# Performance work log

Hardware: AMD Instinct MI355X
Metric: run time of the kernel (lower is better)

The kernel has to match this reference:

```python
import jax, jax.numpy as jnp
import numpy as np

EPS = 1e-8
NEG_INF = -jnp.inf


def setup_inputs() -> dict:
    key = jax.random.key(0)
    k1, k2, k3, k4 = jax.random.split(key, 4)
    B1, S1, B2, S2, H = 64, 128, 64, 128, 768
    x1 = jax.random.normal(k1, (B1, S1, H), dtype=jnp.float32)
    x2 = jax.random.normal(k2, (B2, S2, H), dtype=jnp.float32)
    mask1 = jax.random.randint(k3, (B1, S1), 0, 2).astype(jnp.int32)
    mask2 = jax.random.randint(k4, (B2, S2), 0, 2).astype(jnp.int32)
    # ensure at least one valid token per sequence
    mask1 = mask1.at[:, 0].set(1)
    mask2 = mask2.at[:, 0].set(1)
    return {"x1": x1, "mask1": mask1, "x2": x2, "mask2": mask2}


def _full_cosine(x1, x2):
    # x1: (B1,S1,H), x2: (B2,S2,H) -> sim: (B1,B2,S1,S2)
    n1 = jnp.linalg.norm(x1, axis=-1)  # (B1,S1)
    n2 = jnp.linalg.norm(x2, axis=-1)  # (B2,S2)
    dots = jnp.einsum('ash,bth->abst', x1, x2)
    denom = jnp.maximum(n1[:, None, :, None] * n2[None, :, None, :], EPS)
    return dots / denom


def _masked_mean(sim, mask, axis):
    m = mask.astype(bool)
    num = jnp.sum(jnp.where(m, sim, 0.0), axis=axis)
    den = jnp.sum(mask.astype(sim.dtype), axis=axis)
    return num / den


def reference(x1, mask1, x2, mask2):
    sim = _full_cosine(x1, x2)  # (B1,B2,S1,S2), unmasked cosine
    masked = jnp.where(mask1.astype(bool)[:, None, :, None], sim, NEG_INF)
    masked = jnp.where(mask2.astype(bool)[None, :, None, :], masked, NEG_INF)
    ind1 = jnp.argmax(masked, axis=-1)  # (B1,B2,S1): best x2 token per x1 token
    ind2 = jnp.argmax(masked, axis=-2)  # (B1,B2,S2): best x1 token per x2 token
    # gather unmasked cosine at the argmax indices (equivalent to recomputing
    # cosine on the gathered vectors as the torch code does)
    sim1 = jnp.take_along_axis(sim, ind1[..., None], axis=3)[..., 0]  # (B1,B2,S1)
    sim2 = jnp.take_along_axis(sim, ind2[..., None, :], axis=2)[..., 0, :]  # (B1,B2,S2)
    m1 = jnp.broadcast_to(mask1[:, None, :], sim1.shape)
    m2 = jnp.broadcast_to(mask2[None, :, :], sim2.shape)
    s1 = _masked_mean(sim1, m1, axis=-1)  # (B1,B2)
    s2 = _masked_mean(sim2, m2, axis=-1)  # (B1,B2)
    return (s1 + s2) / 2
```

## Files before the change

### kernel.cpp

```cpp
#include <hip/hip_runtime.h>
#include <hip/hip_bf16.h>

#define H_DIM 768
#define S_LEN 128
#define NT 12
#define MROWS 8192

typedef __attribute__((ext_vector_type(8))) short short8;
typedef __attribute__((ext_vector_type(4))) float f32x4;

__device__ __forceinline__ void gload_lds16(const void* g, void* l) {
  __builtin_amdgcn_global_load_lds(
      (const __attribute__((address_space(1))) unsigned int*)g,
      (__attribute__((address_space(3))) unsigned int*)l, 16, 0, 0);
}

__global__ __launch_bounds__(128) void prep_kernel(
    const int* __restrict__ mask1, const int* __restrict__ mask2,
    int* __restrict__ dest, int* __restrict__ cnts) {
  const int sq = blockIdx.x;
  const int* mask = (sq < 64) ? (mask1 + sq * S_LEN) : (mask2 + (sq - 64) * S_LEN);
  const int tid = threadIdx.x;
  const int lane = tid & 63, wv = tid >> 6;
  const int m = mask[tid] ? 1 : 0;
  const unsigned long long bal = __ballot(m);
  const int pre = __popcll(bal & ((1ull << lane) - 1ull));
  __shared__ int wsum[2];
  if (lane == 0) wsum[wv] = __popcll(bal);
  __syncthreads();
  const int base = (wv == 1) ? wsum[0] : 0;
  dest[sq * S_LEN + tid] = m ? (base + pre) : -1;
  if (tid == 0) cnts[sq] = wsum[0] + wsum[1];
}

__global__ __launch_bounds__(512) void scan_kernel(
    const int* __restrict__ cnts, int* __restrict__ off1, int* __restrict__ off2,
    unsigned* __restrict__ vbitsM, unsigned* __restrict__ vbitsN,
    int* __restrict__ dims) {
  __shared__ int so1[65], so2[65];
  const int tid = threadIdx.x;
  const int lane = tid & 63, wv = tid >> 6;
  if (tid < 128) {
    const int* cb = (wv == 0) ? cnts : (cnts + 64);
    const int np = (cb[lane] + 15) & ~15;
    int inc = np;
#pragma unroll
    for (int o = 1; o < 64; o <<= 1) {
      const int t = __shfl_up(inc, o);
      if (lane >= o) inc += t;
    }
    int* so = wv ? so2 : so1;
    so[lane] = inc - np;
    if (lane == 63) so[64] = inc;
  }
  __syncthreads();
  const int Mtot = so1[64], Ntot = so2[64];
  if (tid == 0) {
    const int Mpad = (Mtot + 127) & ~127, Npad = (Ntot + 127) & ~127;
    dims[0] = Mpad; dims[1] = Npad; dims[2] = Mpad >> 7; dims[3] = Npad >> 7;
  }
  if (tid < 65) { off1[tid] = so1[tid]; off2[tid] = so2[tid]; }
  unsigned bm = 0, bn = 0;
  const int r0 = tid * 16;
  if (r0 < Mtot) {
    int s = 0;
    while (so1[s + 1] <= r0) ++s;
    const int b0 = so1[s], nv = cnts[s];
#pragma unroll
    for (int k = 0; k < 16; ++k)
      if (r0 + k - b0 < nv) bm |= (1u << k);
  }
  if (r0 < Ntot) {
    int s = 0;
    while (so2[s + 1] <= r0) ++s;
    const int b0 = so2[s], nv = cnts[64 + s];
#pragma unroll
    for (int k = 0; k < 16; ++k)
      if (r0 + k - b0 < nv) bn |= (1u << k);
  }
  vbitsM[tid] = bm;
  vbitsN[tid] = bn;
}

__global__ __launch_bounds__(256) void normzero_kernel(
    const float* __restrict__ x1, const float* __restrict__ x2,
    const int* __restrict__ dest, const int* __restrict__ off1,
    const int* __restrict__ off2,
    const unsigned* __restrict__ vbitsM, const unsigned* __restrict__ vbitsN,
    const int* __restrict__ dims,
    unsigned short* __restrict__ xc1, unsigned short* __restrict__ xc2) {
  const int gid = blockIdx.x;
  const int tid = threadIdx.x;
  if (gid >= 16384) {
    const int row = gid - 16384;
    if (tid < 96) {
      const short8 z8 = (short8){0, 0, 0, 0, 0, 0, 0, 0};
      if (row < dims[0] && !((vbitsM[row >> 4] >> (row & 15)) & 1u))
        reinterpret_cast<short8*>(xc1 + (size_t)row * H_DIM)[tid] = z8;
      if (row < dims[1] && !((vbitsN[row >> 4] >> (row & 15)) & 1u))
        reinterpret_cast<short8*>(xc2 + (size_t)row * H_DIM)[tid] = z8;
    }
    return;
  }
  const int sg = gid >> 7, tok = gid & 127;
  const int d = dest[sg * S_LEN + tok];
  if (d < 0) return;
  const bool is1 = (gid < 8192);
  const float* row = is1 ? (x1 + (size_t)gid * H_DIM)
                         : (x2 + (size_t)(gid - 8192) * H_DIM);
  const int grow = (is1 ? off1[sg] : off2[sg - 64]) + d;
  unsigned short* orow = (is1 ? xc1 : xc2) + (size_t)grow * H_DIM;
  float4 v = make_float4(0.f, 0.f, 0.f, 0.f);
  float ss = 0.f;
  if (tid < 192) {
    v = reinterpret_cast<const float4*>(row)[tid];
    ss = v.x * v.x + v.y * v.y + v.z * v.z + v.w * v.w;
  }
#pragma unroll
  for (int o = 32; o > 0; o >>= 1) ss += __shfl_down(ss, o);
  __shared__ float ws[4];
  if ((tid & 63) == 0) ws[tid >> 6] = ss;
  __syncthreads();
  const float scale = 1.0f / sqrtf(ws[0] + ws[1] + ws[2] + ws[3]);
  if (tid < 192) {
    union { ushort4 u; __hip_bfloat16 h[4]; } o;
    o.h[0] = __float2bfloat16(v.x * scale);
    o.h[1] = __float2bfloat16(v.y * scale);
    o.h[2] = __float2bfloat16(v.z * scale);
    o.h[3] = __float2bfloat16(v.w * scale);
    reinterpret_cast<ushort4*>(orow)[tid] = o.u;
  }
}

__global__ __launch_bounds__(256, 4) void gemm_kernel(
    const unsigned short* __restrict__ xc1, const unsigned short* __restrict__ xc2,
    const unsigned* __restrict__ vbitsM, const unsigned* __restrict__ vbitsN,
    const int* __restrict__ dims,
    float* __restrict__ rowgranT, float* __restrict__ colgranT) {
  __shared__ __align__(16) unsigned short Al[128 * 64];
  __shared__ __align__(16) unsigned short Bl[128 * 64];
  const int Nt = dims[3];
  const int nwork = dims[2] * Nt;
  const int bid = blockIdx.x;
  if (bid >= nwork) return;
  const int mt = bid / Nt, nt = bid - mt * Nt;
  const int tid = threadIdx.x;
  const int lane = tid & 63, w = tid >> 6;
  const int wm = w >> 1, wn = w & 1;
  const int g = lane >> 4, rl = lane & 15;
  const unsigned short* A0 = xc1 + (size_t)mt * 128 * H_DIM;
  const unsigned short* B0 = xc2 + (size_t)nt * 128 * H_DIM;

  f32x4 acc[4][4];
#pragma unroll
  for (int i = 0; i < 4; ++i)
#pragma unroll
    for (int j = 0; j < 4; ++j) acc[i][j] = (f32x4){0.f, 0.f, 0.f, 0.f};

  for (int t = 0; t < NT; ++t) {
    __syncthreads();
    const int k0 = t * 64;
#pragma unroll
    for (int q = 0; q < 4; ++q) {
      const int s = q * 256 + tid;
      const int row = s >> 3;
      const int cb = (s & 7) ^ (row & 7);
      gload_lds16(A0 + (size_t)row * H_DIM + k0 + cb * 8, Al + s * 8);
      gload_lds16(B0 + (size_t)row * H_DIM + k0 + cb * 8, Bl + s * 8);
    }
    __syncthreads();
#pragma unroll
    for (int kf = 0; kf < 2; ++kf) {
      const int slot = (kf * 4 + g) ^ (rl & 7);
      short8 av[4], bv[4];
#pragma unroll
      for (int i = 0; i < 4; ++i)
        av[i] = *reinterpret_cast<const short8*>(
            &Al[(wm * 64 + i * 16 + rl) * 64 + slot * 8]);
#pragma unroll
      for (int j = 0; j < 4; ++j)
        bv[j] = *reinterpret_cast<const short8*>(
            &Bl[(wn * 64 + j * 16 + rl) * 64 + slot * 8]);
      __builtin_amdgcn_s_setprio(1);
#pragma unroll
      for (int i = 0; i < 4; ++i)
#pragma unroll
        for (int j = 0; j < 4; ++j)
          acc[i][j] = __builtin_amdgcn_mfma_f32_16x16x32_bf16(
              av[i], bv[j], acc[i][j], 0, 0, 0);
      __builtin_amdgcn_s_setprio(0);
    }
  }

  unsigned bM[4], bN[4];
#pragma unroll
  for (int i = 0; i < 4; ++i) bM[i] = vbitsM[mt * 8 + wm * 4 + i];
#pragma unroll
  for (int j = 0; j < 4; ++j) bN[j] = vbitsN[nt * 8 + wn * 4 + j];

#pragma unroll
  for (int i = 0; i < 4; ++i)
#pragma unroll
    for (int j = 0; j < 4; ++j) {
      const unsigned cvb = bN[j];
#pragma unroll
      for (int r = 0; r < 4; ++r) {
        float pm = ((cvb >> rl) & 1u) ? acc[i][j][r] : -INFINITY;
#pragma unroll
        for (int o = 1; o < 16; o <<= 1) pm = fmaxf(pm, __shfl_xor(pm, o));
        if (rl == 0)
          rowgranT[(size_t)(nt * 8 + wn * 4 + j) * MROWS + mt * 128 + wm * 64 +
                   i * 16 + g * 4 + r] = pm;
      }
    }
#pragma unroll
  for (int i = 0; i < 4; ++i)
#pragma unroll
    for (int j = 0; j < 4; ++j) {
      const unsigned rvb = bM[i];
      float cm = -INFINITY;
#pragma unroll
      for (int r = 0; r < 4; ++r)
        if ((rvb >> (g * 4 + r)) & 1u) cm = fmaxf(cm, acc[i][j][r]);
      cm = fmaxf(cm, __shfl_xor(cm, 16));
      cm = fmaxf(cm, __shfl_xor(cm, 32));
      if (g == 0)
        colgranT[(size_t)(mt * 8 + wm * 4 + i) * MROWS + nt * 128 + wn * 64 +
                 j * 16 + rl] = cm;
    }
}

__global__ __launch_bounds__(128) void reduce_kernel(
    const float* __restrict__ rowgranT, const float* __restrict__ colgranT,
    const int* __restrict__ cnts, const int* __restrict__ off1,
    const int* __restrict__ off2, float* __restrict__ out) {
  const int a = blockIdx.x >> 6, b = blockIdx.x & 63;
  const int n1 = cnts[a], n2 = cnts[64 + b];
  const int o1 = off1[a], o2 = off2[b];
  const int g2s = o2 >> 4, g2n = (n2 + 15) >> 4;
  const int g1s = o1 >> 4, g1n = (n1 + 15) >> 4;
  const int tid = threadIdx.x;
  float v1 = 0.f, v2 = 0.f;
  if (tid < n1) {
    float mx = -INFINITY;
    for (int q = 0; q < g2n; ++q)
      mx = fmaxf(mx, rowgranT[(size_t)(g2s + q) * MROWS + o1 + tid]);
    v1 = mx;
  }
  if (tid < n2) {
    float mx = -INFINITY;
    for (int q = 0; q < g1n; ++q)
      mx = fmaxf(mx, colgranT[(size_t)(g1s + q) * MROWS + o2 + tid]);
    v2 = mx;
  }
#pragma unroll
  for (int o = 32; o > 0; o >>= 1) {
    v1 += __shfl_down(v1, o);
    v2 += __shfl_down(v2, o);
  }
  __shared__ float s1[2], s2[2];
  if ((tid & 63) == 0) { s1[tid >> 6] = v1; s2[tid >> 6] = v2; }
  __syncthreads();
  if (tid == 0)
    out[a * 64 + b] =
        0.5f * ((s1[0] + s1[1]) / (float)n1 + (s2[0] + s2[1]) / (float)n2);
}

extern "C" void kernel_launch(void* const* d_in, const int* in_sizes, int n_in,
                              void* d_out, int out_size, void* d_ws, size_t ws_size,
                              hipStream_t stream) {
  const float* x1 = (const float*)d_in[0];
  const int* mask1 = (const int*)d_in[1];
  const float* x2 = (const float*)d_in[2];
  const int* mask2 = (const int*)d_in[3];
  float* out = (float*)d_out;

  unsigned short* xc1 = (unsigned short*)d_ws;
  unsigned short* xc2 = xc1 + (size_t)8192 * H_DIM;
  float* rowgranT = (float*)(xc2 + (size_t)8192 * H_DIM);
  float* colgranT = rowgranT + (size_t)512 * MROWS;
  int* dest = (int*)(colgranT + (size_t)512 * MROWS);
  int* cnts = dest + 128 * S_LEN;
  int* off1 = cnts + 128;
  int* off2 = off1 + 65;
  unsigned* vbitsM = (unsigned*)(off2 + 65);
  unsigned* vbitsN = vbitsM + 512;
  int* dims = (int*)(vbitsN + 512);

  prep_kernel<<<128, 128, 0, stream>>>(mask1, mask2, dest, cnts);
  scan_kernel<<<1, 512, 0, stream>>>(cnts, off1, off2, vbitsM, vbitsN, dims);
  normzero_kernel<<<24576, 256, 0, stream>>>(x1, x2, dest, off1, off2, vbitsM,
                                             vbitsN, dims, xc1, xc2);
  gemm_kernel<<<4096, 256, 0, stream>>>(xc1, xc2, vbitsM, vbitsN, dims,
                                        rowgranT, colgranT);
  reduce_kernel<<<4096, 128, 0, stream>>>(rowgranT, colgranT, cnts, off1, off2,
                                          out);
}
```

Baseline: 93.40 us.

## Pre-pack bf16 operands into MFMA fragment layout and load directly from global

Result: no change. 94.17 us (+0.8%).

```diff
diff --git a/kernel.cpp b/kernel.cpp
--- a/kernel.cpp
+++ b/kernel.cpp
@@ -3,17 +3,10 @@
 
 #define H_DIM 768
 #define S_LEN 128
-#define NT 12
 #define MROWS 8192
 
 typedef __attribute__((ext_vector_type(8))) short short8;
 typedef __attribute__((ext_vector_type(4))) float f32x4;
-
-__device__ __forceinline__ void gload_lds16(const void* g, void* l) {
-  __builtin_amdgcn_global_load_lds(
-      (const __attribute__((address_space(1))) unsigned int*)g,
-      (__attribute__((address_space(3))) unsigned int*)l, 16, 0, 0);
-}
 
 __global__ __launch_bounds__(128) void prep_kernel(
     const int* __restrict__ mask1, const int* __restrict__ mask2,
@@ -88,17 +81,18 @@
     const int* __restrict__ off2,
     const unsigned* __restrict__ vbitsM, const unsigned* __restrict__ vbitsN,
     const int* __restrict__ dims,
-    unsigned short* __restrict__ xc1, unsigned short* __restrict__ xc2) {
+    unsigned short* __restrict__ xc1p, unsigned short* __restrict__ xc2p) {
   const int gid = blockIdx.x;
   const int tid = threadIdx.x;
   if (gid >= 16384) {
     const int row = gid - 16384;
     if (tid < 96) {
       const short8 z8 = (short8){0, 0, 0, 0, 0, 0, 0, 0};
+      const size_t base = ((size_t)(row >> 4) * 96 + tid) * 128 + (row & 15) * 8;
       if (row < dims[0] && !((vbitsM[row >> 4] >> (row & 15)) & 1u))
-        reinterpret_cast<short8*>(xc1 + (size_t)row * H_DIM)[tid] = z8;
+        *reinterpret_cast<short8*>(xc1p + base) = z8;
       if (row < dims[1] && !((vbitsN[row >> 4] >> (row & 15)) & 1u))
-        reinterpret_cast<short8*>(xc2 + (size_t)row * H_DIM)[tid] = z8;
+        *reinterpret_cast<short8*>(xc2p + base) = z8;
     }
     return;
   }
@@ -109,7 +103,7 @@
   const float* row = is1 ? (x1 + (size_t)gid * H_DIM)
                          : (x2 + (size_t)(gid - 8192) * H_DIM);
   const int grow = (is1 ? off1[sg] : off2[sg - 64]) + d;
-  unsigned short* orow = (is1 ? xc1 : xc2) + (size_t)grow * H_DIM;
+  unsigned short* xp = is1 ? xc1p : xc2p;
   float4 v = make_float4(0.f, 0.f, 0.f, 0.f);
   float ss = 0.f;
   if (tid < 192) {
@@ -128,17 +122,17 @@
     o.h[1] = __float2bfloat16(v.y * scale);
     o.h[2] = __float2bfloat16(v.z * scale);
     o.h[3] = __float2bfloat16(v.w * scale);
-    reinterpret_cast<ushort4*>(orow)[tid] = o.u;
+    const size_t addr = ((size_t)(grow >> 4) * 96 + (tid >> 1)) * 128 +
+                        (grow & 15) * 8 + (tid & 1) * 4;
+    *reinterpret_cast<ushort4*>(xp + addr) = o.u;
   }
 }
 
 __global__ __launch_bounds__(256, 4) void gemm_kernel(
-    const unsigned short* __restrict__ xc1, const unsigned short* __restrict__ xc2,
+    const unsigned short* __restrict__ xc1p, const unsigned short* __restrict__ xc2p,
     const unsigned* __restrict__ vbitsM, const unsigned* __restrict__ vbitsN,
     const int* __restrict__ dims,
     float* __restrict__ rowgranT, float* __restrict__ colgranT) {
-  __shared__ __align__(16) unsigned short Al[128 * 64];
-  __shared__ __align__(16) unsigned short Bl[128 * 64];
   const int Nt = dims[3];
   const int nwork = dims[2] * Nt;
   const int bid = blockIdx.x;
@@ -148,8 +142,16 @@
   const int lane = tid & 63, w = tid >> 6;
   const int wm = w >> 1, wn = w & 1;
   const int g = lane >> 4, rl = lane & 15;
-  const unsigned short* A0 = xc1 + (size_t)mt * 128 * H_DIM;
-  const unsigned short* B0 = xc2 + (size_t)nt * 128 * H_DIM;
+  const int laneoff = g * 128 + rl * 8;
+
+  const unsigned short* Ab0 = xc1p + (size_t)(mt * 8 + wm * 4 + 0) * 12288 + laneoff;
+  const unsigned short* Ab1 = xc1p + (size_t)(mt * 8 + wm * 4 + 1) * 12288 + laneoff;
+  const unsigned short* Ab2 = xc1p + (size_t)(mt * 8 + wm * 4 + 2) * 12288 + laneoff;
+  const unsigned short* Ab3 = xc1p + (size_t)(mt * 8 + wm * 4 + 3) * 12288 + laneoff;
+  const unsigned short* Bb0 = xc2p + (size_t)(nt * 8 + wn * 4 + 0) * 12288 + laneoff;
+  const unsigned short* Bb1 = xc2p + (size_t)(nt * 8 + wn * 4 + 1) * 12288 + laneoff;
+  const unsigned short* Bb2 = xc2p + (size_t)(nt * 8 + wn * 4 + 2) * 12288 + laneoff;
+  const unsigned short* Bb3 = xc2p + (size_t)(nt * 8 + wn * 4 + 3) * 12288 + laneoff;
 
   f32x4 acc[4][4];
 #pragma unroll
@@ -157,39 +159,26 @@
 #pragma unroll
     for (int j = 0; j < 4; ++j) acc[i][j] = (f32x4){0.f, 0.f, 0.f, 0.f};
 
-  for (int t = 0; t < NT; ++t) {
-    __syncthreads();
-    const int k0 = t * 64;
-#pragma unroll
-    for (int q = 0; q < 4; ++q) {
-      const int s = q * 256 + tid;
-      const int row = s >> 3;
-      const int cb = (s & 7) ^ (row & 7);
-      gload_lds16(A0 + (size_t)row * H_DIM + k0 + cb * 8, Al + s * 8);
-      gload_lds16(B0 + (size_t)row * H_DIM + k0 + cb * 8, Bl + s * 8);
-    }
-    __syncthreads();
-#pragma unroll
-    for (int kf = 0; kf < 2; ++kf) {
-      const int slot = (kf * 4 + g) ^ (rl & 7);
-      short8 av[4], bv[4];
-#pragma unroll
-      for (int i = 0; i < 4; ++i)
-        av[i] = *reinterpret_cast<const short8*>(
-            &Al[(wm * 64 + i * 16 + rl) * 64 + slot * 8]);
+#pragma unroll 4
+  for (int s = 0; s < 24; ++s) {
+    const int off = s * 512;
+    short8 av[4], bv[4];
+    av[0] = *reinterpret_cast<const short8*>(Ab0 + off);
+    av[1] = *reinterpret_cast<const short8*>(Ab1 + off);
+    av[2] = *reinterpret_cast<const short8*>(Ab2 + off);
+    av[3] = *reinterpret_cast<const short8*>(Ab3 + off);
+    bv[0] = *reinterpret_cast<const short8*>(Bb0 + off);
+    bv[1] = *reinterpret_cast<const short8*>(Bb1 + off);
+    bv[2] = *reinterpret_cast<const short8*>(Bb2 + off);
+    bv[3] = *reinterpret_cast<const short8*>(Bb3 + off);
+    __builtin_amdgcn_s_setprio(1);
+#pragma unroll
+    for (int i = 0; i < 4; ++i)
 #pragma unroll
       for (int j = 0; j < 4; ++j)
-        bv[j] = *reinterpret_cast<const short8*>(
-            &Bl[(wn * 64 + j * 16 + rl) * 64 + slot * 8]);
-      __builtin_amdgcn_s_setprio(1);
-#pragma unroll
-      for (int i = 0; i < 4; ++i)
-#pragma unroll
-        for (int j = 0; j < 4; ++j)
-          acc[i][j] = __builtin_amdgcn_mfma_f32_16x16x32_bf16(
-              av[i], bv[j], acc[i][j], 0, 0, 0);
-      __builtin_amdgcn_s_setprio(0);
-    }
+        acc[i][j] = __builtin_amdgcn_mfma_f32_16x16x32_bf16(
+            av[i], bv[j], acc[i][j], 0, 0, 0);
+    __builtin_amdgcn_s_setprio(0);
   }
 
   unsigned bM[4], bN[4];
@@ -275,9 +264,9 @@
   const int* mask2 = (const int*)d_in[3];
   float* out = (float*)d_out;
 
-  unsigned short* xc1 = (unsigned short*)d_ws;
-  unsigned short* xc2 = xc1 + (size_t)8192 * H_DIM;
-  float* rowgranT = (float*)(xc2 + (size_t)8192 * H_DIM);
+  unsigned short* xc1p = (unsigned short*)d_ws;
+  unsigned short* xc2p = xc1p + (size_t)8192 * H_DIM;
+  float* rowgranT = (float*)(xc2p + (size_t)8192 * H_DIM);
   float* colgranT = rowgranT + (size_t)512 * MROWS;
   int* dest = (int*)(colgranT + (size_t)512 * MROWS);
   int* cnts = dest + 128 * S_LEN;
@@ -290,8 +279,8 @@
   prep_kernel<<<128, 128, 0, stream>>>(mask1, mask2, dest, cnts);
   scan_kernel<<<1, 512, 0, stream>>>(cnts, off1, off2, vbitsM, vbitsN, dims);
   normzero_kernel<<<24576, 256, 0, stream>>>(x1, x2, dest, off1, off2, vbitsM,
-                                             vbitsN, dims, xc1, xc2);
-  gemm_kernel<<<4096, 256, 0, stream>>>(xc1, xc2, vbitsM, vbitsN, dims,
+                                             vbitsN, dims, xc1p, xc2p);
+  gemm_kernel<<<4096, 256, 0, stream>>>(xc1p, xc2p, vbitsM, vbitsN, dims,
                                         rowgranT, colgranT);
   reduce_kernel<<<4096, 128, 0, stream>>>(rowgranT, colgranT, cnts, off1, off2,
                                           out);
```
